# Kernel optimization log

Measured on AMD Instinct MI355X. Metric: run time of the kernel, lower is better.

## Reference

```python
import jax, jax.numpy as jnp
import numpy as np

B, S, D = 4, 2048, 1024
E = 8
H = int(D * 2.5)  # 2560


def setup_inputs() -> dict:
    key = jax.random.key(0)
    ks = jax.random.split(key, 6)
    scale = 0.02
    x = jax.random.normal(ks[0], (B, S, D), dtype=jnp.float32)
    Wr = jax.random.normal(ks[1], (E, D), dtype=jnp.float32) * scale   # router: logits = x @ Wr.T
    Wg = jax.random.normal(ks[2], (E, H, D), dtype=jnp.float32) * scale  # gate proj per expert
    Wu = jax.random.normal(ks[3], (E, H, D), dtype=jnp.float32) * scale  # up proj per expert
    Wd = jax.random.normal(ks[4], (E, D, H), dtype=jnp.float32) * scale  # down proj per expert
    return {"x": x, "Wr": Wr, "Wg": Wg, "Wu": Wu, "Wd": Wd, "top_k": 2}


def reference(x, Wr, Wg, Wu, Wd, top_k):
    num_experts = Wg.shape[0]
    logits = jnp.einsum('bsd,ed->bse', x, Wr)              # [B,S,E]
    probs = jax.nn.softmax(logits, axis=-1)
    k = min(top_k, num_experts)
    topv, topi = jax.lax.top_k(probs, k)                   # [B,S,k]
    out = jnp.zeros_like(x)
    for ei in range(num_experts):
        mask = jnp.any(topi == ei, axis=-1)                # [B,S] bool
        h = jax.nn.silu(jnp.einsum('bsd,hd->bsh', x, Wg[ei])) \
            * jnp.einsum('bsd,hd->bsh', x, Wu[ei])         # [B,S,H]
        ex = jnp.einsum('bsh,dh->bsd', h, Wd[ei])          # [B,S,D]
        w = (probs[..., ei] * mask.astype(x.dtype))[..., None]
        out = out + ex * w
    return (out, logits, probs, topi)
```

## Files before the change

### kernel.cpp

```cpp
#include <hip/hip_runtime.h>

#define T_TOK 8192
#define DD    1024
#define EE    8
#define HH    2560
#define PAIR_CAP (T_TOK*2 + 128)
#define MT_MAX 64
#define NT1   (HH/64)
#define NT2   (DD/128)

typedef __attribute__((ext_vector_type(8))) short bf16x8;
typedef __attribute__((ext_vector_type(4))) float f32x4;

__device__ __forceinline__ unsigned short f2b(float f) {
  union { float f; unsigned u; } v; v.f = f;
  unsigned r = v.u + 0x7FFFu + ((v.u >> 16) & 1u);
  return (unsigned short)(r >> 16);
}

__device__ __forceinline__ void async16(const void* g, void* l) {
  __builtin_amdgcn_global_load_lds(
      (const __attribute__((address_space(1))) unsigned int*)(unsigned long long)g,
      (__attribute__((address_space(3))) unsigned int*)l,
      16, 0, 0);
}

__global__ void zero_ints(int* a, int n) {
  int i = threadIdx.x;
  if (i < n) a[i] = 0;
}

__global__ void conv_bf16(const float* __restrict__ s, unsigned short* __restrict__ d, int n4) {
  int i = blockIdx.x * blockDim.x + threadIdx.x;
  if (i >= n4) return;
  float4 v = ((const float4*)s)[i];
  ushort4 o;
  o.x = f2b(v.x); o.y = f2b(v.y); o.z = f2b(v.z); o.w = f2b(v.w);
  ((ushort4*)d)[i] = o;
}

__global__ __launch_bounds__(256) void router(
    const float* __restrict__ x, const float* __restrict__ Wr,
    unsigned short* __restrict__ xb,
    float* __restrict__ o_logits, float* __restrict__ o_probs, float* __restrict__ o_topi,
    int* __restrict__ top_e, float* __restrict__ top_p, int* __restrict__ counts)
{
  __shared__ float sWr[EE * DD];
  int tid = threadIdx.x;
  const float4* w4 = (const float4*)Wr;
  float4* s4 = (float4*)sWr;
  for (int i = tid; i < EE * DD / 4; i += 256) s4[i] = w4[i];
  __syncthreads();

  int wv = tid >> 6, lane = tid & 63;
  int t = blockIdx.x * 4 + wv;
  const float4* xt4 = (const float4*)(x + (size_t)t * DD);
  ushort4* xbt = (ushort4*)(xb + (size_t)t * DD);

  float acc[EE];
#pragma unroll
  for (int e = 0; e < EE; e++) acc[e] = 0.f;
#pragma unroll
  for (int p = 0; p < 4; p++) {
    float4 v = xt4[p * 64 + lane];
    ushort4 o;
    o.x = f2b(v.x); o.y = f2b(v.y); o.z = f2b(v.z); o.w = f2b(v.w);
    xbt[p * 64 + lane] = o;
    int d = (p * 64 + lane) * 4;
#pragma unroll
    for (int e = 0; e < EE; e++) {
      const float* wr = &sWr[e * DD + d];
      acc[e] += v.x * wr[0] + v.y * wr[1] + v.z * wr[2] + v.w * wr[3];
    }
  }
#pragma unroll
  for (int e = 0; e < EE; e++) {
#pragma unroll
    for (int off = 32; off; off >>= 1) acc[e] += __shfl_down(acc[e], off);
  }
  if (lane == 0) {
    float mx = acc[0];
#pragma unroll
    for (int e = 1; e < EE; e++) mx = fmaxf(mx, acc[e]);
    float p[EE]; float sum = 0.f;
#pragma unroll
    for (int e = 0; e < EE; e++) { p[e] = __expf(acc[e] - mx); sum += p[e]; }
    float inv = 1.f / sum;
#pragma unroll
    for (int e = 0; e < EE; e++) {
      p[e] *= inv;
      o_logits[(size_t)t * EE + e] = acc[e];
      o_probs [(size_t)t * EE + e] = p[e];
    }
    int i0 = 0;
#pragma unroll
    for (int e = 1; e < EE; e++) if (p[e] > p[i0]) i0 = e;
    int i1 = (i0 == 0) ? 1 : 0;
#pragma unroll
    for (int e = 0; e < EE; e++) if (e != i0 && p[e] > p[i1]) i1 = e;

    o_topi[t * 2 + 0] = (float)i0;
    o_topi[t * 2 + 1] = (float)i1;
    top_e[t * 2 + 0] = i0; top_e[t * 2 + 1] = i1;
    top_p[t * 2 + 0] = p[i0]; top_p[t * 2 + 1] = p[i1];
    atomicAdd(&counts[i0], 1);
    atomicAdd(&counts[i1], 1);
  }
}

__global__ void mk_offsets(const int* __restrict__ counts, int* __restrict__ offsets,
                           int* __restrict__ cursors) {
  if (threadIdx.x == 0) {
    int s = 0;
    for (int e = 0; e < EE; e++) { offsets[e] = s; s += counts[e]; }
  }
  if (threadIdx.x < EE) cursors[threadIdx.x] = 0;
}

__global__ void scatter(const int* __restrict__ top_e,
                        const int* __restrict__ offsets, int* __restrict__ cursors,
                        int* __restrict__ list, int* __restrict__ slot) {
  int t = blockIdx.x * blockDim.x + threadIdx.x;
  if (t >= T_TOK) return;
#pragma unroll
  for (int k = 0; k < 2; k++) {
    int e = top_e[t * 2 + k];
    int pos = atomicAdd(&cursors[e], 1);
    int dst = offsets[e] + pos;
    list[dst] = t;
    slot[t * 2 + k] = dst;
  }
}

__global__ __launch_bounds__(256) void gemm_gateup(
    const unsigned short* __restrict__ xb,
    const unsigned short* __restrict__ Wgb,
    const unsigned short* __restrict__ Wub,
    const int* __restrict__ list, const int* __restrict__ offsets,
    const int* __restrict__ counts,
    unsigned short* __restrict__ hbuf)
{
  int bx = blockIdx.x;
  int e = bx / (MT_MAX * NT1);
  int rem = bx - e * (MT_MAX * NT1);
  int mt = rem / NT1;
  int nt = rem - mt * NT1;
  int n_e = counts[e];
  if (mt * 128 >= n_e) return;
  int off_e = offsets[e];

  __shared__ unsigned short sA [2][128 * 32];
  __shared__ unsigned short sBg[2][ 64 * 32];
  __shared__ unsigned short sBu[2][ 64 * 32];

  int tid = threadIdx.x, wv = tid >> 6, lane = tid & 63;
  const unsigned short* wg_e = Wgb + (size_t)e * HH * DD;
  const unsigned short* wu_e = Wub + (size_t)e * HH * DD;

  size_t aBase[2];
#pragma unroll
  for (int i = 0; i < 2; i++) {
    int c = i * 256 + tid;
    int r = c >> 2, j = c & 3;
    int jj = j ^ ((r >> 1) & 3);
    int idx = mt * 128 + r;
    if (idx >= n_e) idx = n_e - 1;
    int tok = list[off_e + idx];
    aBase[i] = (size_t)tok * DD + (size_t)(jj * 8);
  }
  size_t bBase;
  {
    int r = tid >> 2, j = tid & 3;
    int jj = j ^ ((r >> 1) & 3);
    bBase = (size_t)(nt * 64 + r) * DD + (size_t)(jj * 8);
  }

  f32x4 accg[4][2] = {};
  f32x4 accu[4][2] = {};
  int wm = (wv >> 1) * 64, wn = (wv & 1) * 32;

  auto stage = [&](int b, int k0) {
    async16(xb  + aBase[0] + k0, &sA [b][(      wv * 64) * 8]);
    async16(xb  + aBase[1] + k0, &sA [b][(256 + wv * 64) * 8]);
    async16(wg_e + bBase   + k0, &sBg[b][(      wv * 64) * 8]);
    async16(wu_e + bBase   + k0, &sBu[b][(      wv * 64) * 8]);
  };

  stage(0, 0);
  int cur = 0;
  int q = lane >> 4;
  for (int k0 = 0; k0 < DD; k0 += 32) {
    __syncthreads();
    if (k0 + 32 < DD) stage(cur ^ 1, k0 + 32);

    bf16x8 af[4], bg[2], bu[2];
#pragma unroll
    for (int fi = 0; fi < 4; fi++) {
      int r = wm + fi * 16 + (lane & 15);
      int ch = q ^ ((r >> 1) & 3);
      af[fi] = *(const bf16x8*)&sA[cur][r * 32 + ch * 8];
    }
#pragma unroll
    for (int fj = 0; fj < 2; fj++) {
      int r = wn + fj * 16 + (lane & 15);
      int ch = q ^ ((r >> 1) & 3);
      bg[fj] = *(const bf16x8*)&sBg[cur][r * 32 + ch * 8];
      bu[fj] = *(const bf16x8*)&sBu[cur][r * 32 + ch * 8];
    }
#pragma unroll
    for (int fi = 0; fi < 4; fi++)
#pragma unroll
      for (int fj = 0; fj < 2; fj++) {
        accg[fi][fj] = __builtin_amdgcn_mfma_f32_16x16x32_bf16(af[fi], bg[fj], accg[fi][fj], 0, 0, 0);
        accu[fi][fj] = __builtin_amdgcn_mfma_f32_16x16x32_bf16(af[fi], bu[fj], accu[fi][fj], 0, 0, 0);
      }
    cur ^= 1;
  }

#pragma unroll
  for (int fi = 0; fi < 4; fi++) {
    int mBase = mt * 128 + wm + fi * 16 + ((lane >> 4) << 2);
#pragma unroll
    for (int fj = 0; fj < 2; fj++) {
      int col = nt * 64 + wn + fj * 16 + (lane & 15);
#pragma unroll
      for (int r = 0; r < 4; r++) {
        int m = mBase + r;
        if (m < n_e) {
          float g = accg[fi][fj][r];
          float u = accu[fi][fj][r];
          float hv = g / (1.f + __expf(-g)) * u;
          hbuf[(size_t)(off_e + m) * HH + col] = f2b(hv);
        }
      }
    }
  }
}

__global__ __launch_bounds__(256) void gemm_down(
    const unsigned short* __restrict__ hbuf,
    const unsigned short* __restrict__ Wdb,
    const int* __restrict__ offsets,
    const int* __restrict__ counts,
    float* __restrict__ tmp)
{
  int bx = blockIdx.x;
  int e = bx / (MT_MAX * NT2);
  int rem = bx - e * (MT_MAX * NT2);
  int mt = rem / NT2;
  int nt = rem - mt * NT2;
  int n_e = counts[e];
  if (mt * 128 >= n_e) return;
  int off_e = offsets[e];

  __shared__ unsigned short sA[2][128 * 32];
  __shared__ unsigned short sB[2][128 * 32];
  int tid = threadIdx.x, wv = tid >> 6, lane = tid & 63;
  const unsigned short* wd_e = Wdb + (size_t)e * DD * HH;

  size_t aBase[2], bBase[2];
#pragma unroll
  for (int i = 0; i < 2; i++) {
    int c = i * 256 + tid;
    int r = c >> 2, j = c & 3;
    int jj = j ^ ((r >> 1) & 3);
    aBase[i] = (size_t)(off_e + mt * 128 + r) * HH + (size_t)(jj * 8);
    bBase[i] = (size_t)(nt * 128 + r) * HH + (size_t)(jj * 8);
  }

  f32x4 acc[4][4] = {};
  int wm = (wv >> 1) * 64, wn = (wv & 1) * 64;

  auto stage = [&](int b, int k0) {
    async16(hbuf + aBase[0] + k0, &sA[b][(      wv * 64) * 8]);
    async16(hbuf + aBase[1] + k0, &sA[b][(256 + wv * 64) * 8]);
    async16(wd_e + bBase[0] + k0, &sB[b][(      wv * 64) * 8]);
    async16(wd_e + bBase[1] + k0, &sB[b][(256 + wv * 64) * 8]);
  };

  stage(0, 0);
  int cur = 0;
  int q = lane >> 4;
  for (int k0 = 0; k0 < HH; k0 += 32) {
    __syncthreads();
    if (k0 + 32 < HH) stage(cur ^ 1, k0 + 32);

    bf16x8 af[4], bfr[4];
#pragma unroll
    for (int f = 0; f < 4; f++) {
      int ra = wm + f * 16 + (lane & 15);
      int ca = q ^ ((ra >> 1) & 3);
      af[f] = *(const bf16x8*)&sA[cur][ra * 32 + ca * 8];
      int rb = wn + f * 16 + (lane & 15);
      int cb = q ^ ((rb >> 1) & 3);
      bfr[f] = *(const bf16x8*)&sB[cur][rb * 32 + cb * 8];
    }
#pragma unroll
    for (int fi = 0; fi < 4; fi++)
#pragma unroll
      for (int fj = 0; fj < 4; fj++)
        acc[fi][fj] = __builtin_amdgcn_mfma_f32_16x16x32_bf16(af[fi], bfr[fj], acc[fi][fj], 0, 0, 0);
    cur ^= 1;
  }

#pragma unroll
  for (int fi = 0; fi < 4; fi++) {
    int mBase = mt * 128 + wm + fi * 16 + ((lane >> 4) << 2);
#pragma unroll
    for (int r = 0; r < 4; r++) {
      int m = mBase + r;
      if (m < n_e) {
        float* orow = tmp + (size_t)(off_e + m) * DD + nt * 128 + wn;
#pragma unroll
        for (int fj = 0; fj < 4; fj++)
          orow[fj * 16 + (lane & 15)] = acc[fi][fj][r];
      }
    }
  }
}

__global__ __launch_bounds__(256) void combine(
    const float* __restrict__ tmp, const int* __restrict__ slot,
    const float* __restrict__ top_p, float* __restrict__ out)
{
  int t = blockIdx.x, d = threadIdx.x;
  int s0 = slot[t * 2 + 0], s1 = slot[t * 2 + 1];
  float p0 = top_p[t * 2 + 0], p1 = top_p[t * 2 + 1];
  float4 a = ((const float4*)(tmp + (size_t)s0 * DD))[d];
  float4 b = ((const float4*)(tmp + (size_t)s1 * DD))[d];
  float4 o;
  o.x = p0 * a.x + p1 * b.x;
  o.y = p0 * a.y + p1 * b.y;
  o.z = p0 * a.z + p1 * b.z;
  o.w = p0 * a.w + p1 * b.w;
  ((float4*)(out + (size_t)t * DD))[d] = o;
}

extern "C" void kernel_launch(void* const* d_in, const int* in_sizes, int n_in,
                              void* d_out, int out_size, void* d_ws, size_t ws_size,
                              hipStream_t stream) {
  const float* x  = (const float*)d_in[0];
  const float* Wr = (const float*)d_in[1];
  const float* Wg = (const float*)d_in[2];
  const float* Wu = (const float*)d_in[3];
  const float* Wd = (const float*)d_in[4];

  float* out      = (float*)d_out;
  float* o_logits = out + (size_t)T_TOK * DD;
  float* o_probs  = o_logits + (size_t)T_TOK * EE;
  float* o_topi   = o_probs + (size_t)T_TOK * EE;

  char* w = (char*)d_ws;
  auto alloc = [&](size_t bytes) {
    char* p = w;
    w += (bytes + 255) & ~(size_t)255;
    return p;
  };
  unsigned short* Wgb = (unsigned short*)alloc((size_t)EE * HH * DD * 2);
  unsigned short* Wub = (unsigned short*)alloc((size_t)EE * HH * DD * 2);
  unsigned short* Wdb = (unsigned short*)alloc((size_t)EE * DD * HH * 2);
  unsigned short* xb  = (unsigned short*)alloc((size_t)T_TOK * DD * 2);
  unsigned short* hb  = (unsigned short*)alloc((size_t)PAIR_CAP * HH * 2);
  int*   top_e   = (int*)  alloc((size_t)T_TOK * 2 * 4);
  float* top_p   = (float*)alloc((size_t)T_TOK * 2 * 4);
  int*   counts  = (int*)  alloc(64);
  int*   offsets = (int*)  alloc(64);
  int*   cursors = (int*)  alloc(64);
  int*   list    = (int*)  alloc((size_t)PAIR_CAP * 4);
  int*   slot    = (int*)  alloc((size_t)T_TOK * 2 * 4);

  float* tmp = (float*)Wgb;

  zero_ints<<<1, 64, 0, stream>>>(counts, EE);
  {
    int nw4 = EE * HH * DD / 4;
    conv_bf16<<<(nw4 + 255) / 256, 256, 0, stream>>>(Wg, Wgb, nw4);
    conv_bf16<<<(nw4 + 255) / 256, 256, 0, stream>>>(Wu, Wub, nw4);
    conv_bf16<<<(nw4 + 255) / 256, 256, 0, stream>>>(Wd, Wdb, nw4);
  }
  router<<<T_TOK / 4, 256, 0, stream>>>(x, Wr, xb, o_logits, o_probs, o_topi, top_e, top_p, counts);
  mk_offsets<<<1, 64, 0, stream>>>(counts, offsets, cursors);
  scatter<<<T_TOK / 256, 256, 0, stream>>>(top_e, offsets, cursors, list, slot);
  gemm_gateup<<<EE * MT_MAX * NT1, 256, 0, stream>>>(xb, Wgb, Wub, list, offsets, counts, hb);
  gemm_down<<<EE * MT_MAX * NT2, 256, 0, stream>>>(hb, Wdb, offsets, counts, tmp);
  combine<<<T_TOK, 256, 0, stream>>>(tmp, slot, top_p, out);
}
```

Baseline: 983.0 us.

## Keep two LDS stages in flight with explicit vmcnt waits; fuse weight conversions

Both expert GEMMs now prefetch two k-tiles ahead and wait with an explicit vmcnt count instead of a full __syncthreads. Each tile is read into registers before a barrier, and the freed buffer is then refilled, so global loads overlap more of the MFMA work. MFMA issue priority is raised with s_setprio. The three weight fp32-to-bf16 conversion launches are merged into one launch with a 3-wide grid y dimension. The hand-written waitcnt values depend on the exact number of async loads issued per stage, which makes the code fragile if the staging changes.

```diff
diff --git a/kernel.cpp b/kernel.cpp
--- a/kernel.cpp
+++ b/kernel.cpp
@@ -30,9 +30,14 @@
   if (i < n) a[i] = 0;
 }
 
-__global__ void conv_bf16(const float* __restrict__ s, unsigned short* __restrict__ d, int n4) {
+__global__ void conv_bf16_3(const float* __restrict__ s0, const float* __restrict__ s1,
+                            const float* __restrict__ s2,
+                            unsigned short* __restrict__ d0, unsigned short* __restrict__ d1,
+                            unsigned short* __restrict__ d2, int n4) {
   int i = blockIdx.x * blockDim.x + threadIdx.x;
   if (i >= n4) return;
+  const float* s = (blockIdx.y == 0) ? s0 : (blockIdx.y == 1) ? s1 : s2;
+  unsigned short* d = (blockIdx.y == 0) ? d0 : (blockIdx.y == 1) ? d1 : d2;
   float4 v = ((const float4*)s)[i];
   ushort4 o;
   o.x = f2b(v.x); o.y = f2b(v.y); o.z = f2b(v.z); o.w = f2b(v.w);
@@ -186,12 +191,15 @@
     async16(wu_e + bBase   + k0, &sBu[b][(      wv * 64) * 8]);
   };
 
+  const int NK = DD / 32;
   stage(0, 0);
-  int cur = 0;
+  stage(1, 32);
   int q = lane >> 4;
-  for (int k0 = 0; k0 < DD; k0 += 32) {
-    __syncthreads();
-    if (k0 + 32 < DD) stage(cur ^ 1, k0 + 32);
+  for (int t = 0; t < NK; ++t) {
+    int cur = t & 1;
+    if (t == NK - 1) asm volatile("s_waitcnt vmcnt(0)" ::: "memory");
+    else             asm volatile("s_waitcnt vmcnt(4)" ::: "memory");
+    __builtin_amdgcn_s_barrier();
 
     bf16x8 af[4], bg[2], bu[2];
 #pragma unroll
@@ -207,6 +215,12 @@
       bg[fj] = *(const bf16x8*)&sBg[cur][r * 32 + ch * 8];
       bu[fj] = *(const bf16x8*)&sBu[cur][r * 32 + ch * 8];
     }
+    asm volatile("s_waitcnt lgkmcnt(0)" ::: "memory");
+    __builtin_amdgcn_sched_barrier(0);
+    __builtin_amdgcn_s_barrier();
+    if (t + 2 < NK) stage(cur, (t + 2) * 32);
+
+    __builtin_amdgcn_s_setprio(1);
 #pragma unroll
     for (int fi = 0; fi < 4; fi++)
 #pragma unroll
@@ -214,7 +228,7 @@
         accg[fi][fj] = __builtin_amdgcn_mfma_f32_16x16x32_bf16(af[fi], bg[fj], accg[fi][fj], 0, 0, 0);
         accu[fi][fj] = __builtin_amdgcn_mfma_f32_16x16x32_bf16(af[fi], bu[fj], accu[fi][fj], 0, 0, 0);
       }
-    cur ^= 1;
+    __builtin_amdgcn_s_setprio(0);
   }
 
 #pragma unroll
@@ -278,12 +292,15 @@
     async16(wd_e + bBase[1] + k0, &sB[b][(256 + wv * 64) * 8]);
   };
 
+  const int NK = HH / 32;
   stage(0, 0);
-  int cur = 0;
+  stage(1, 32);
   int q = lane >> 4;
-  for (int k0 = 0; k0 < HH; k0 += 32) {
-    __syncthreads();
-    if (k0 + 32 < HH) stage(cur ^ 1, k0 + 32);
+  for (int t = 0; t < NK; ++t) {
+    int cur = t & 1;
+    if (t == NK - 1) asm volatile("s_waitcnt vmcnt(0)" ::: "memory");
+    else             asm volatile("s_waitcnt vmcnt(4)" ::: "memory");
+    __builtin_amdgcn_s_barrier();
 
     bf16x8 af[4], bfr[4];
 #pragma unroll
@@ -295,12 +312,18 @@
       int cb = q ^ ((rb >> 1) & 3);
       bfr[f] = *(const bf16x8*)&sB[cur][rb * 32 + cb * 8];
     }
+    asm volatile("s_waitcnt lgkmcnt(0)" ::: "memory");
+    __builtin_amdgcn_sched_barrier(0);
+    __builtin_amdgcn_s_barrier();
+    if (t + 2 < NK) stage(cur, (t + 2) * 32);
+
+    __builtin_amdgcn_s_setprio(1);
 #pragma unroll
     for (int fi = 0; fi < 4; fi++)
 #pragma unroll
       for (int fj = 0; fj < 4; fj++)
         acc[fi][fj] = __builtin_amdgcn_mfma_f32_16x16x32_bf16(af[fi], bfr[fj], acc[fi][fj], 0, 0, 0);
-    cur ^= 1;
+    __builtin_amdgcn_s_setprio(0);
   }
 
 #pragma unroll
@@ -374,9 +397,8 @@
   zero_ints<<<1, 64, 0, stream>>>(counts, EE);
   {
     int nw4 = EE * HH * DD / 4;
-    conv_bf16<<<(nw4 + 255) / 256, 256, 0, stream>>>(Wg, Wgb, nw4);
-    conv_bf16<<<(nw4 + 255) / 256, 256, 0, stream>>>(Wu, Wub, nw4);
-    conv_bf16<<<(nw4 + 255) / 256, 256, 0, stream>>>(Wd, Wdb, nw4);
+    dim3 g((nw4 + 255) / 256, 3);
+    conv_bf16_3<<<g, 256, 0, stream>>>(Wg, Wu, Wd, Wgb, Wub, Wdb, nw4);
   }
   router<<<T_TOK / 4, 256, 0, stream>>>(x, Wr, xb, o_logits, o_probs, o_topi, top_e, top_p, counts);
   mk_offsets<<<1, 64, 0, stream>>>(counts, offsets, cursors);
```

Measured after the change: 899.4 us. -8.5%, faster.
